# Performance work log

Measured on AMD Instinct MI355X. Metric: run time of the kernel, lower is better.

Reference implementation:

```python
import jax, jax.numpy as jnp
import numpy as np

B, N, D = 8, 1024, 768
H = 12
HD = D // H  # 64
SCALE = HD ** (-0.5)


def setup_inputs() -> dict:
    key = jax.random.key(0)
    ks = jax.random.split(key, 11)
    s = 0.02
    return {
        "x": jax.random.normal(ks[0], (B, N, D), dtype=jnp.float32),
        "w_q": jax.random.normal(ks[1], (D, D), dtype=jnp.float32) * s,
        "b_q": jax.random.normal(ks[2], (D,), dtype=jnp.float32) * s,
        "w_k": jax.random.normal(ks[3], (D, D), dtype=jnp.float32) * s,
        "b_k": jax.random.normal(ks[4], (D,), dtype=jnp.float32) * s,
        "w_v": jax.random.normal(ks[5], (D, D), dtype=jnp.float32) * s,
        "b_v": jax.random.normal(ks[6], (D,), dtype=jnp.float32) * s,
        "w_qt": jax.random.normal(ks[7], (D, D), dtype=jnp.float32) * s,
        "b_qt": jax.random.normal(ks[8], (D,), dtype=jnp.float32) * s,
        "w_p": jax.random.normal(ks[9], (D, D), dtype=jnp.float32) * s,
        "b_p": jax.random.normal(ks[10], (D,), dtype=jnp.float32) * s,
    }


def _heads(y):
    # [B,N,D] -> [B,H,N,HD]
    b, n, d = y.shape
    return y.reshape(b, n, H, HD).transpose(0, 2, 1, 3)


def reference(x, w_q, b_q, w_k, b_k, w_v, b_v, w_qt, b_qt, w_p, b_p):
    # torch nn.Linear: y = x @ W.T + b
    q = _heads(x @ w_q.T + b_q)
    k = _heads(x @ w_k.T + b_k)
    v = _heads(x @ w_v.T + b_v)
    q_tilde = _heads(x @ w_qt.T + b_qt)
    # NOTE: source divides by self.scale = head_dim**-0.5 (i.e. multiplies by sqrt(hd)); reproduced faithfully
    corr = jnp.einsum("bhnd,bhmd->bhnm", q_tilde, k) / SCALE
    scores = jnp.einsum("bhnd,bhmd->bhnm", q, k) / SCALE + corr
    attn = jax.nn.softmax(scores, axis=-1)
    out = jnp.einsum("bhnm,bhmd->bhnd", attn, v)  # [B,H,N,HD]
    out = out.transpose(0, 2, 1, 3).reshape(x.shape[0], x.shape[1], D)
    out = out @ w_p.T + b_p
    return out, corr
```

## Files before the change

kernel.cpp:

```cpp
#include <hip/hip_runtime.h>

typedef __bf16 bf16_t;
typedef __bf16 bf16x8 __attribute__((ext_vector_type(8)));
typedef __bf16 bf16x4 __attribute__((ext_vector_type(4)));
typedef float f32x4 __attribute__((ext_vector_type(4)));

constexpr int BATCH = 8;
constexpr int NSEQ = 1024;
constexpr int DMODEL = 768;
constexpr int NH = 12;
constexpr int HDIM = 64;
constexpr int MROWS = BATCH * NSEQ;
constexpr int WSZ = DMODEL * DMODEL;
constexpr float L2E = 1.44269504088896f;

#define AS1(p) ((const __attribute__((address_space(1))) void*)(p))
#define AS3(p) ((__attribute__((address_space(3))) void*)(p))

__global__ __launch_bounds__(256) void prep_w(
    const float* __restrict__ wq, const float* __restrict__ wqt,
    const float* __restrict__ wk, const float* __restrict__ wv,
    const float* __restrict__ wp, const float* __restrict__ bq,
    const float* __restrict__ bqt, ushort* __restrict__ wb_,
    float* __restrict__ bqs)
{
    int i = blockIdx.x * 256 + threadIdx.x;
    bf16_t* w = (bf16_t*)wb_;
    float a = wq[i], b = wqt[i];
    w[i]            = (bf16_t)(a + b);
    w[WSZ + i]      = (bf16_t)b;
    w[2*WSZ + i]    = (bf16_t)wk[i];
    w[3*WSZ + i]    = (bf16_t)wv[i];
    w[4*WSZ + i]    = (bf16_t)wp[i];
    if (i < DMODEL) bqs[i] = bq[i] + bqt[i];
}

__global__ __launch_bounds__(256) void conv_x(const float* __restrict__ x,
                                              ushort* __restrict__ xb_)
{
    int i = (blockIdx.x * 256 + threadIdx.x) * 4;
    float4 v = *(const float4*)(x + i);
    bf16x4 r = { (bf16_t)v.x, (bf16_t)v.y, (bf16_t)v.z, (bf16_t)v.w };
    *(bf16x4*)((bf16_t*)xb_ + i) = r;
}

__device__ __forceinline__ void gemm_core(
    const bf16_t* __restrict__ A, const bf16_t* __restrict__ W,
    bf16_t* As, bf16_t* Bs, int m0, int n0, int tid, f32x4 acc[4][4])
{
    const int lane = tid & 63, wave = tid >> 6;
    const int g = lane >> 4, c = lane & 15;
    const int wm = wave >> 1, wn = wave & 1;

    const int r_b = tid >> 3;
    const int koff = 8 * ((tid & 7) ^ (r_b & 7));
    const size_t arow = (size_t)(m0 + r_b) * DMODEL + koff;
    const size_t brow = (size_t)(n0 + r_b) * DMODEL + koff;
    char* As_base = (char*)As + (tid & ~63) * 16;
    char* Bs_base = (char*)Bs + (tid & ~63) * 16;

    for (int k0 = 0; k0 < DMODEL; k0 += 64) {
        __syncthreads();
#pragma unroll
        for (int i = 0; i < 4; i++)
            __builtin_amdgcn_global_load_lds(
                AS1(A + arow + k0 + (size_t)i * 32 * DMODEL),
                AS3(As_base + i * 4096), 16, 0, 0);
#pragma unroll
        for (int i = 0; i < 4; i++)
            __builtin_amdgcn_global_load_lds(
                AS1(W + brow + k0 + (size_t)i * 32 * DMODEL),
                AS3(Bs_base + i * 4096), 16, 0, 0);
        __syncthreads();
#pragma unroll
        for (int kk = 0; kk < 2; kk++) {
            bf16x8 af[4], bfr[4];
#pragma unroll
            for (int mt = 0; mt < 4; mt++) {
                int r = wm * 64 + mt * 16 + c;
                af[mt] = *(const bf16x8*)(As + r * 64 + ((kk * 4 + g) ^ (r & 7)) * 8);
            }
#pragma unroll
            for (int nt = 0; nt < 4; nt++) {
                int r = wn * 64 + nt * 16 + c;
                bfr[nt] = *(const bf16x8*)(Bs + r * 64 + ((kk * 4 + g) ^ (r & 7)) * 8);
            }
#pragma unroll
            for (int mt = 0; mt < 4; mt++)
#pragma unroll
                for (int nt = 0; nt < 4; nt++)
                    acc[mt][nt] = __builtin_amdgcn_mfma_f32_16x16x32_bf16(
                        af[mt], bfr[nt], acc[mt][nt], 0, 0, 0);
        }
    }
}

__global__ __launch_bounds__(256) void gemm_qkv(
    const ushort* __restrict__ xb_, const ushort* __restrict__ wb_,
    const float* __restrict__ bqs, const float* __restrict__ bqt,
    const float* __restrict__ bk, const float* __restrict__ bv,
    ushort* __restrict__ o0, ushort* __restrict__ o1,
    ushort* __restrict__ o2, ushort* __restrict__ o3)
{
    __shared__ alignas(16) bf16_t As[128 * 64];
    __shared__ alignas(16) bf16_t Bs[128 * 64];
    const int z = blockIdx.z;
    const bf16_t* A = (const bf16_t*)xb_;
    const bf16_t* W = (const bf16_t*)wb_ + (size_t)z * WSZ;
    const float* bias = (z == 0) ? bqs : (z == 1) ? bqt : (z == 2) ? bk : bv;
    bf16_t* outp = (bf16_t*)((z == 0) ? o0 : (z == 1) ? o1 : (z == 2) ? o2 : o3);
    const int m0 = blockIdx.x * 128, n0 = blockIdx.y * 128;
    f32x4 acc[4][4] = {};
    gemm_core(A, W, As, Bs, m0, n0, threadIdx.x, acc);

    const int tid = threadIdx.x, lane = tid & 63, wave = tid >> 6;
    const int g = lane >> 4, c = lane & 15;
    const int wm = wave >> 1, wn = wave & 1;
#pragma unroll
    for (int mt = 0; mt < 4; mt++)
#pragma unroll
        for (int nt = 0; nt < 4; nt++) {
            int col = n0 + wn * 64 + nt * 16 + c;
            int h = col >> 6, hd = col & 63;
            float bsv = bias[col];
#pragma unroll
            for (int j = 0; j < 4; j++) {
                int row = m0 + wm * 64 + mt * 16 + 4 * g + j;
                int b = row >> 10, ns = row & 1023;
                outp[(((size_t)b * NH + h) * NSEQ + ns) * HDIM + hd] =
                    (bf16_t)(acc[mt][nt][j] + bsv);
            }
        }
}

__global__ __launch_bounds__(256) void gemm_out(
    const ushort* __restrict__ ao_, const ushort* __restrict__ wp_,
    const float* __restrict__ bp, float* __restrict__ out)
{
    __shared__ alignas(16) bf16_t As[128 * 64];
    __shared__ alignas(16) bf16_t Bs[128 * 64];
    const bf16_t* A = (const bf16_t*)ao_;
    const bf16_t* W = (const bf16_t*)wp_;
    const int m0 = blockIdx.x * 128, n0 = blockIdx.y * 128;
    f32x4 acc[4][4] = {};
    gemm_core(A, W, As, Bs, m0, n0, threadIdx.x, acc);

    const int tid = threadIdx.x, lane = tid & 63, wave = tid >> 6;
    const int g = lane >> 4, c = lane & 15;
    const int wm = wave >> 1, wn = wave & 1;
#pragma unroll
    for (int mt = 0; mt < 4; mt++)
#pragma unroll
        for (int nt = 0; nt < 4; nt++) {
            int col = n0 + wn * 64 + nt * 16 + c;
            float bsv = bp[col];
#pragma unroll
            for (int j = 0; j < 4; j++) {
                int row = m0 + wm * 64 + mt * 16 + 4 * g + j;
                out[(size_t)row * DMODEL + col] = acc[mt][nt][j] + bsv;
            }
        }
}

__global__ __launch_bounds__(256) void attn_kernel(
    const ushort* __restrict__ qs_, const ushort* __restrict__ qt_,
    const ushort* __restrict__ kb_, const ushort* __restrict__ vb_,
    ushort* __restrict__ ao_, float* __restrict__ corr)
{
    __shared__ alignas(16) bf16_t VT[64 * 64];
    __shared__ alignas(16) bf16_t P[4][16 * 72];
    const bf16_t* QS = (const bf16_t*)qs_;
    const bf16_t* QT = (const bf16_t*)qt_;
    const bf16_t* Kb = (const bf16_t*)kb_;
    const bf16_t* Vb = (const bf16_t*)vb_;
    bf16_t* Ob = (bf16_t*)ao_;

    const int tid = threadIdx.x;
    const int w = tid >> 6, lane = tid & 63;
    const int g = lane >> 4, c = lane & 15;
    const int bh = blockIdx.x >> 4, qb = blockIdx.x & 15;
    const int q0 = qb * 64 + w * 16;
    const size_t base = (size_t)bh * (NSEQ * HDIM);

    bf16x8 qsf[2], qtf[2];
#pragma unroll
    for (int kk = 0; kk < 2; kk++) {
        qsf[kk] = *(const bf16x8*)(QS + base + (size_t)(q0 + c) * HDIM + kk * 32 + 8 * g);
        qtf[kk] = *(const bf16x8*)(QT + base + (size_t)(q0 + c) * HDIM + kk * 32 + 8 * g);
    }
    f32x4 oacc[4] = {};
    float mrun[4], lrun[4];
#pragma unroll
    for (int j = 0; j < 4; j++) { mrun[j] = -3e30f; lrun[j] = 0.f; }

    float* corr_b = corr + (size_t)bh * (NSEQ * NSEQ);

    for (int t = 0; t < 16; t++) {
        const int kv0 = t * 64;
        __syncthreads();
#pragma unroll
        for (int r2 = 0; r2 < 2; r2++) {
            const int hd0 = (r2 * 4 + w) * 8;
            bf16x8 vv = *(const bf16x8*)(Vb + base + (size_t)(kv0 + lane) * HDIM + hd0);
#pragma unroll
            for (int e = 0; e < 8; e++) {
                const int hd = hd0 + e;
                VT[hd * 64 + (lane ^ ((hd & 7) << 3))] = vv[e];
            }
        }
        f32x4 sv[4];
#pragma unroll
        for (int kvt = 0; kvt < 4; kvt++) {
            const size_t krow = base + (size_t)(kv0 + kvt * 16 + c) * HDIM + 8 * g;
            bf16x8 kf0 = *(const bf16x8*)(Kb + krow);
            bf16x8 kf1 = *(const bf16x8*)(Kb + krow + 32);
            f32x4 sa = {0.f, 0.f, 0.f, 0.f};
            f32x4 ca = {0.f, 0.f, 0.f, 0.f};
            sa = __builtin_amdgcn_mfma_f32_16x16x32_bf16(qsf[0], kf0, sa, 0, 0, 0);
            sa = __builtin_amdgcn_mfma_f32_16x16x32_bf16(qsf[1], kf1, sa, 0, 0, 0);
            ca = __builtin_amdgcn_mfma_f32_16x16x32_bf16(qtf[0], kf0, ca, 0, 0, 0);
            ca = __builtin_amdgcn_mfma_f32_16x16x32_bf16(qtf[1], kf1, ca, 0, 0, 0);
            sv[kvt] = sa * 8.0f;
            ca = ca * 8.0f;
#pragma unroll
            for (int j = 0; j < 4; j++)
                __builtin_nontemporal_store(
                    ca[j],
                    &corr_b[(size_t)(q0 + 4 * g + j) * NSEQ + kv0 + kvt * 16 + c]);
        }
        float mn[4], sc[4], ps[4];
#pragma unroll
        for (int j = 0; j < 4; j++) {
            float tm = fmaxf(fmaxf(sv[0][j], sv[1][j]), fmaxf(sv[2][j], sv[3][j]));
            tm = fmaxf(tm, __shfl_xor(tm, 1));
            tm = fmaxf(tm, __shfl_xor(tm, 2));
            tm = fmaxf(tm, __shfl_xor(tm, 4));
            tm = fmaxf(tm, __shfl_xor(tm, 8));
            mn[j] = fmaxf(mrun[j], tm);
            sc[j] = exp2f((mrun[j] - mn[j]) * L2E);
            mrun[j] = mn[j];
            ps[j] = 0.f;
        }
#pragma unroll
        for (int kvt = 0; kvt < 4; kvt++)
#pragma unroll
            for (int j = 0; j < 4; j++) {
                float p = exp2f((sv[kvt][j] - mn[j]) * L2E);
                sv[kvt][j] = p;
                ps[j] += p;
            }
#pragma unroll
        for (int j = 0; j < 4; j++) {
            float s = ps[j];
            s += __shfl_xor(s, 1);
            s += __shfl_xor(s, 2);
            s += __shfl_xor(s, 4);
            s += __shfl_xor(s, 8);
            lrun[j] = lrun[j] * sc[j] + s;
#pragma unroll
            for (int nt = 0; nt < 4; nt++) oacc[nt][j] *= sc[j];
        }
#pragma unroll
        for (int kvt = 0; kvt < 4; kvt++)
#pragma unroll
            for (int j = 0; j < 4; j++)
                P[w][(4 * g + j) * 72 + kvt * 16 + c] = (bf16_t)sv[kvt][j];
        __syncthreads();
#pragma unroll
        for (int kk = 0; kk < 2; kk++) {
            bf16x8 pa = *(const bf16x8*)(&P[w][c * 72 + kk * 32 + 8 * g]);
#pragma unroll
            for (int nt = 0; nt < 4; nt++) {
                const int hd = nt * 16 + c;
                bf16x8 vf = *(const bf16x8*)(&VT[hd * 64 + ((kk * 32 + 8 * g) ^ ((hd & 7) << 3))]);
                oacc[nt] = __builtin_amdgcn_mfma_f32_16x16x32_bf16(pa, vf, oacc[nt], 0, 0, 0);
            }
        }
    }
    const int b = bh / NH, h = bh % NH;
#pragma unroll
    for (int nt = 0; nt < 4; nt++)
#pragma unroll
        for (int j = 0; j < 4; j++) {
            float val = oacc[nt][j] / lrun[j];
            Ob[(size_t)(b * NSEQ + q0 + 4 * g + j) * DMODEL + h * HDIM + nt * 16 + c] =
                (bf16_t)val;
        }
}

extern "C" void kernel_launch(void* const* d_in, const int* in_sizes, int n_in,
                              void* d_out, int out_size, void* d_ws, size_t ws_size,
                              hipStream_t stream)
{
    const float* x   = (const float*)d_in[0];
    const float* wq  = (const float*)d_in[1];
    const float* bq  = (const float*)d_in[2];
    const float* wk  = (const float*)d_in[3];
    const float* bk  = (const float*)d_in[4];
    const float* wv  = (const float*)d_in[5];
    const float* bv  = (const float*)d_in[6];
    const float* wqt = (const float*)d_in[7];
    const float* bqt = (const float*)d_in[8];
    const float* wp  = (const float*)d_in[9];
    const float* bp  = (const float*)d_in[10];

    char* ws = (char*)d_ws;
    ushort* xb  = (ushort*)(ws);
    ushort* wb  = (ushort*)(ws + 12582912);
    float*  bqs = (float*)(ws + 18481152);
    ushort* qs  = (ushort*)(ws + 18485248);
    ushort* qt  = qs + 6291456;
    ushort* kb  = qt + 6291456;
    ushort* vb  = kb + 6291456;
    ushort* ao  = vb + 6291456;

    float* out  = (float*)d_out;
    float* corr = out + (size_t)6291456;

    prep_w<<<2304, 256, 0, stream>>>(wq, wqt, wk, wv, wp, bq, bqt, wb, bqs);
    conv_x<<<6144, 256, 0, stream>>>(x, xb);
    gemm_qkv<<<dim3(64, 6, 4), 256, 0, stream>>>(xb, wb, bqs, bqt, bk, bv,
                                                 qs, qt, kb, vb);
    attn_kernel<<<1536, 256, 0, stream>>>(qs, qt, kb, vb, ao, corr);
    gemm_out<<<dim3(64, 6), 256, 0, stream>>>(ao, wb + (size_t)4 * WSZ, bp, out);
}
```

Baseline: 272.4 us.

## Remap blocks for XCD locality, double-buffer V tile, vectorize corr stores

```diff
diff --git a/kernel.cpp b/kernel.cpp
--- a/kernel.cpp
+++ b/kernel.cpp
@@ -104,12 +104,16 @@
 {
     __shared__ alignas(16) bf16_t As[128 * 64];
     __shared__ alignas(16) bf16_t Bs[128 * 64];
-    const int z = blockIdx.z;
+    const int bid = blockIdx.x;
+    const int gid = (bid & 7) * 192 + (bid >> 3);
+    const int z = gid / 384;
+    const int rr = gid % 384;
+    const int m0 = (rr / 6) * 128, n0 = (rr % 6) * 128;
+
     const bf16_t* A = (const bf16_t*)xb_;
     const bf16_t* W = (const bf16_t*)wb_ + (size_t)z * WSZ;
     const float* bias = (z == 0) ? bqs : (z == 1) ? bqt : (z == 2) ? bk : bv;
     bf16_t* outp = (bf16_t*)((z == 0) ? o0 : (z == 1) ? o1 : (z == 2) ? o2 : o3);
-    const int m0 = blockIdx.x * 128, n0 = blockIdx.y * 128;
     f32x4 acc[4][4] = {};
     gemm_core(A, W, As, Bs, m0, n0, threadIdx.x, acc);
 
@@ -139,9 +143,12 @@
 {
     __shared__ alignas(16) bf16_t As[128 * 64];
     __shared__ alignas(16) bf16_t Bs[128 * 64];
+    const int bid = blockIdx.x;
+    const int gid = (bid & 7) * 48 + (bid >> 3);
+    const int m0 = (gid / 6) * 128, n0 = (gid % 6) * 128;
+
     const bf16_t* A = (const bf16_t*)ao_;
     const bf16_t* W = (const bf16_t*)wp_;
-    const int m0 = blockIdx.x * 128, n0 = blockIdx.y * 128;
     f32x4 acc[4][4] = {};
     gemm_core(A, W, As, Bs, m0, n0, threadIdx.x, acc);
 
@@ -167,7 +174,7 @@
     const ushort* __restrict__ kb_, const ushort* __restrict__ vb_,
     ushort* __restrict__ ao_, float* __restrict__ corr)
 {
-    __shared__ alignas(16) bf16_t VT[64 * 64];
+    __shared__ alignas(16) bf16_t VT[2][64 * 64];
     __shared__ alignas(16) bf16_t P[4][16 * 72];
     const bf16_t* QS = (const bf16_t*)qs_;
     const bf16_t* QT = (const bf16_t*)qt_;
@@ -178,7 +185,9 @@
     const int tid = threadIdx.x;
     const int w = tid >> 6, lane = tid & 63;
     const int g = lane >> 4, c = lane & 15;
-    const int bh = blockIdx.x >> 4, qb = blockIdx.x & 15;
+    const int bid = blockIdx.x;
+    const int gid = (bid & 7) * 192 + (bid >> 3);
+    const int bh = gid >> 4, qb = gid & 15;
     const int q0 = qb * 64 + w * 16;
     const size_t base = (size_t)bh * (NSEQ * HDIM);
 
@@ -197,7 +206,7 @@
 
     for (int t = 0; t < 16; t++) {
         const int kv0 = t * 64;
-        __syncthreads();
+        bf16_t* vt = VT[t & 1];
 #pragma unroll
         for (int r2 = 0; r2 < 2; r2++) {
             const int hd0 = (r2 * 4 + w) * 8;
@@ -205,7 +214,7 @@
 #pragma unroll
             for (int e = 0; e < 8; e++) {
                 const int hd = hd0 + e;
-                VT[hd * 64 + (lane ^ ((hd & 7) << 3))] = vv[e];
+                vt[hd * 64 + (lane ^ ((hd & 7) << 3))] = vv[e];
             }
         }
         f32x4 sv[4];
@@ -218,15 +227,12 @@
             f32x4 ca = {0.f, 0.f, 0.f, 0.f};
             sa = __builtin_amdgcn_mfma_f32_16x16x32_bf16(qsf[0], kf0, sa, 0, 0, 0);
             sa = __builtin_amdgcn_mfma_f32_16x16x32_bf16(qsf[1], kf1, sa, 0, 0, 0);
-            ca = __builtin_amdgcn_mfma_f32_16x16x32_bf16(qtf[0], kf0, ca, 0, 0, 0);
-            ca = __builtin_amdgcn_mfma_f32_16x16x32_bf16(qtf[1], kf1, ca, 0, 0, 0);
+            ca = __builtin_amdgcn_mfma_f32_16x16x32_bf16(kf0, qtf[0], ca, 0, 0, 0);
+            ca = __builtin_amdgcn_mfma_f32_16x16x32_bf16(kf1, qtf[1], ca, 0, 0, 0);
             sv[kvt] = sa * 8.0f;
             ca = ca * 8.0f;
-#pragma unroll
-            for (int j = 0; j < 4; j++)
-                __builtin_nontemporal_store(
-                    ca[j],
-                    &corr_b[(size_t)(q0 + 4 * g + j) * NSEQ + kv0 + kvt * 16 + c]);
+            __builtin_nontemporal_store(
+                ca, (f32x4*)(corr_b + (size_t)(q0 + c) * NSEQ + kv0 + kvt * 16 + 4 * g));
         }
         float mn[4], sc[4], ps[4];
 #pragma unroll
@@ -272,7 +278,7 @@
 #pragma unroll
             for (int nt = 0; nt < 4; nt++) {
                 const int hd = nt * 16 + c;
-                bf16x8 vf = *(const bf16x8*)(&VT[hd * 64 + ((kk * 32 + 8 * g) ^ ((hd & 7) << 3))]);
+                bf16x8 vf = *(const bf16x8*)(&vt[hd * 64 + ((kk * 32 + 8 * g) ^ ((hd & 7) << 3))]);
                 oacc[nt] = __builtin_amdgcn_mfma_f32_16x16x32_bf16(pa, vf, oacc[nt], 0, 0, 0);
             }
         }
@@ -319,8 +325,7 @@
 
     prep_w<<<2304, 256, 0, stream>>>(wq, wqt, wk, wv, wp, bq, bqt, wb, bqs);
     conv_x<<<6144, 256, 0, stream>>>(x, xb);
-    gemm_qkv<<<dim3(64, 6, 4), 256, 0, stream>>>(xb, wb, bqs, bqt, bk, bv,
-                                                 qs, qt, kb, vb);
+    gemm_qkv<<<1536, 256, 0, stream>>>(xb, wb, bqs, bqt, bk, bv, qs, qt, kb, vb);
     attn_kernel<<<1536, 256, 0, stream>>>(qs, qt, kb, vb, ao, corr);
-    gemm_out<<<dim3(64, 6), 256, 0, stream>>>(ao, wb + (size_t)4 * WSZ, bp, out);
-}
+    gemm_out<<<384, 256, 0, stream>>>(ao, wb + (size_t)4 * WSZ, bp, out);
+}
```

Result: slower. 285.6 us (+4.9%).
